# Optimization experiments

Measured on AMD Instinct MI355X. Metric: run time of the kernel, lower is better.

Reference implementation:

```python
import jax, jax.numpy as jnp
import numpy as np

D_HEAD = 64
IGNORE = -100000.0


def setup_inputs() -> dict:
    key = jax.random.key(0)
    ks = jax.random.split(key, 5)
    B, S, D, H, M = 2, 2048, 768, 12, D_HEAD
    scale = 0.05  # 'random_normal' keras init stddev
    return {
        "x": jax.random.normal(ks[0], (B, S, D), jnp.float32),
        "W_Q": jax.random.normal(ks[1], (H, D, M), jnp.float32) * scale,
        "b_Q": jnp.zeros((H, M), jnp.float32),
        "W_K": jax.random.normal(ks[2], (H, D, M), jnp.float32) * scale,
        "b_K": jnp.zeros((H, M), jnp.float32),
        "W_V": jax.random.normal(ks[3], (H, D, M), jnp.float32) * scale,
        "b_V": jnp.zeros((H, M), jnp.float32),
        "W_O": jax.random.normal(ks[4], (H, M, D), jnp.float32) * scale,
        "b_O": jnp.zeros((D,), jnp.float32),
    }


def reference(x, W_Q, b_Q, W_K, b_K, W_V, b_V, W_O, b_O):
    # q,k,v: [b, s, h, m]
    q = jnp.einsum("bqd,hdm->bqhm", x, W_Q) + b_Q
    k = jnp.einsum("bkd,hdm->bkhm", x, W_K) + b_K
    v = jnp.einsum("bkd,hdm->bkhm", x, W_V) + b_V
    # scores: [b, h, q, k], scaled by 1/sqrt(d_head)
    scores = jnp.einsum("bqhm,bkhm->bhqk", q, k) / jnp.sqrt(
        jnp.asarray(D_HEAD, q.dtype)
    )
    S = x.shape[1]
    # causal mask: strictly-upper-triangular positions set to IGNORE (-1e5),
    # matching tf.where(mask == 1, IGNORE, scores)
    causal = jnp.arange(S)[:, None] >= jnp.arange(S)[None, :]  # [q, k]
    scores = jnp.where(causal[None, None, :, :], scores, jnp.asarray(IGNORE, scores.dtype))
    pattern = jax.nn.softmax(scores, axis=-1)
    z = jnp.einsum("bhqk,bkhm->bqhm", pattern, v)
    attn_out = jnp.einsum("bqhm,hmd->bqd", z, W_O) + b_O
    return attn_out
```

## Files before the change

### kernel.cpp

```cpp
#include <hip/hip_runtime.h>
#include <hip/hip_bf16.h>
#include <cstdint>
#include <cstddef>

#define B_ 2
#define S_ 2048
#define D_ 768
#define H_ 12
#define M_ 64
#define BS_ (B_ * S_)
#define NQKV_ 2304
#define NCHUNK_ 80
#define TOTCHUNK_ (24 * NCHUNK_)
#define QSCALE 0.18033688011f

typedef __attribute__((ext_vector_type(8))) short bf16x8;
typedef __attribute__((ext_vector_type(4))) short bf16x4;
typedef __attribute__((ext_vector_type(4))) float f32x4;

__device__ __forceinline__ unsigned short f2bu(float f) {
    __hip_bfloat16 h = __float2bfloat16(f);
    unsigned short u;
    __builtin_memcpy(&u, &h, 2);
    return u;
}
__device__ __forceinline__ unsigned pack2(float a, float b) {
    return (unsigned)f2bu(a) | ((unsigned)f2bu(b) << 16);
}

__device__ __forceinline__ bf16x8 ld16(const unsigned short* p) {
    p = (const unsigned short*)__builtin_assume_aligned(p, 16);
    bf16x8 v; __builtin_memcpy(&v, p, 16); return v;
}
__device__ __forceinline__ bf16x4 ld8(const unsigned short* p) {
    p = (const unsigned short*)__builtin_assume_aligned(p, 8);
    bf16x4 v; __builtin_memcpy(&v, p, 8); return v;
}
__device__ __forceinline__ uint4 ld16u(const unsigned short* p) {
    p = (const unsigned short*)__builtin_assume_aligned(p, 16);
    uint4 v; __builtin_memcpy(&v, p, 16); return v;
}
__device__ __forceinline__ void st16(unsigned short* p, uint4 v) {
    p = (unsigned short*)__builtin_assume_aligned(p, 16);
    __builtin_memcpy(p, &v, 16);
}
__device__ __forceinline__ void st8(unsigned short* p, uint2 v) {
    p = (unsigned short*)__builtin_assume_aligned(p, 8);
    __builtin_memcpy(p, &v, 8);
}
__device__ __forceinline__ float4 ldf4(const float* p) {
    p = (const float*)__builtin_assume_aligned(p, 16);
    float4 v; __builtin_memcpy(&v, p, 16); return v;
}
__device__ __forceinline__ void async16(const unsigned short* g, unsigned short* l) {
    __builtin_amdgcn_global_load_lds(
        (const __attribute__((address_space(1))) void*)g,
        (__attribute__((address_space(3))) void*)l, 16, 0, 0);
}
__device__ __forceinline__ void b82f(uint4 u, float* o) {
    o[0] = __uint_as_float(u.x << 16); o[1] = __uint_as_float(u.x & 0xffff0000u);
    o[2] = __uint_as_float(u.y << 16); o[3] = __uint_as_float(u.y & 0xffff0000u);
    o[4] = __uint_as_float(u.z << 16); o[5] = __uint_as_float(u.z & 0xffff0000u);
    o[6] = __uint_as_float(u.w << 16); o[7] = __uint_as_float(u.w & 0xffff0000u);
}

#define NEG_BIG (-3.0e38f)

__global__ void prep(const float* __restrict__ WQ, const float* __restrict__ WK,
                     const float* __restrict__ WV, const float* __restrict__ WO,
                     const float* __restrict__ x,
                     unsigned short* __restrict__ WT,
                     unsigned short* __restrict__ WOT,
                     unsigned short* __restrict__ xb)
{
    const int bx = blockIdx.x;
    if (bx < 216) {
        const int xx = bx % 9, yy = bx / 9;
        const int c  = xx * 256 + threadIdx.x;
        const int k0 = yy * 32;
        const int which = c / D_;
        const int r = c - which * D_;
        const int h = r >> 6, m = r & 63;
        const float* Wsel = (which == 0) ? WQ : (which == 1) ? WK : WV;
        const float* src = Wsel + (size_t)h * D_ * M_ + m;
        unsigned short* dst = WT + (size_t)c * D_ + k0;
        for (int i = 0; i < 32; i += 8) {
            float wv[8];
#pragma unroll
            for (int j = 0; j < 8; j++) wv[j] = src[(size_t)(k0 + i + j) * M_];
            uint4 pu;
            pu.x = pack2(wv[0], wv[1]); pu.y = pack2(wv[2], wv[3]);
            pu.z = pack2(wv[4], wv[5]); pu.w = pack2(wv[6], wv[7]);
            st16(dst + i, pu);
        }
    } else if (bx < 288) {
        const int b2 = bx - 216;
        const int xx = b2 % 3, yy = b2 / 3;
        const int c  = xx * 256 + threadIdx.x;
        const int k0 = yy * 32;
        unsigned short* dst = WOT + (size_t)c * D_ + k0;
        for (int i = 0; i < 32; i += 8) {
            float wv[8];
#pragma unroll
            for (int j = 0; j < 8; j++) wv[j] = WO[(size_t)(k0 + i + j) * D_ + c];
            uint4 pu;
            pu.x = pack2(wv[0], wv[1]); pu.y = pack2(wv[2], wv[3]);
            pu.z = pack2(wv[4], wv[5]); pu.w = pack2(wv[6], wv[7]);
            st16(dst + i, pu);
        }
    } else {
        const size_t i = ((size_t)(bx - 288) * 256 + threadIdx.x) * 16;
#pragma unroll
        for (int p = 0; p < 2; p++) {
            float4 a0 = ldf4(x + i + p * 8), a1 = ldf4(x + i + p * 8 + 4);
            uint4 u;
            u.x = pack2(a0.x, a0.y); u.y = pack2(a0.z, a0.w);
            u.z = pack2(a1.x, a1.y); u.w = pack2(a1.z, a1.w);
            st16(xb + i + p * 8, u);
        }
    }
}

__global__ __launch_bounds__(256, 2) void qkv_gemm(
    const unsigned short* __restrict__ xb,
    const unsigned short* __restrict__ WT,
    const float* __restrict__ bQ, const float* __restrict__ bK,
    const float* __restrict__ bV,
    unsigned short* __restrict__ qo, unsigned short* __restrict__ ko,
    unsigned short* __restrict__ vt)
{
    const int row0 = blockIdx.x * 128;
    const int col0 = blockIdx.y * 128;
    const int t = threadIdx.x;
    const int w = t >> 6, lane = t & 63, quad = lane >> 4, l16 = lane & 15;
    const int wrow0 = (w & 1) * 64, wcol0 = (w >> 1) * 64;

    __shared__ unsigned short Alds[128 * 64];
    __shared__ unsigned short Blds[128 * 64];

    f32x4 acc[4][4] = {};

    const unsigned short* asrc[4];
    const unsigned short* bsrc[4];
    int ldsoff[4];
#pragma unroll
    for (int q = 0; q < 4; q++) {
        const int cq = w * 256 + q * 64 + lane;
        const int row = cq >> 3, c = cq & 7;
        const int cs = c ^ (row & 7);
        asrc[q] = xb + (size_t)(row0 + row) * D_ + cs * 8;
        bsrc[q] = WT + (size_t)(col0 + row) * D_ + cs * 8;
        ldsoff[q] = (w * 256 + q * 64) * 8;
    }
    const int swz = (l16 & 7);

    for (int k0 = 0; k0 < D_; k0 += 64) {
#pragma unroll
        for (int q = 0; q < 4; q++) async16(asrc[q] + k0, Alds + ldsoff[q]);
#pragma unroll
        for (int q = 0; q < 4; q++) async16(bsrc[q] + k0, Blds + ldsoff[q]);
        __syncthreads();

        bf16x8 af[4][2], bfm[4][2];
#pragma unroll
        for (int rt = 0; rt < 4; rt++) {
            const int row = wrow0 + rt * 16 + l16;
#pragma unroll
            for (int hh = 0; hh < 2; hh++)
                af[rt][hh] = ld16(&Alds[row * 64 + ((hh * 4 + quad) ^ swz) * 8]);
        }
#pragma unroll
        for (int st = 0; st < 4; st++) {
            const int row = wcol0 + st * 16 + l16;
#pragma unroll
            for (int hh = 0; hh < 2; hh++)
                bfm[st][hh] = ld16(&Blds[row * 64 + ((hh * 4 + quad) ^ swz) * 8]);
        }
#pragma unroll
        for (int rt = 0; rt < 4; rt++)
#pragma unroll
            for (int st = 0; st < 4; st++) {
                acc[rt][st] = __builtin_amdgcn_mfma_f32_16x16x32_bf16(
                    af[rt][0], bfm[st][0], acc[rt][st], 0, 0, 0);
                acc[rt][st] = __builtin_amdgcn_mfma_f32_16x16x32_bf16(
                    af[rt][1], bfm[st][1], acc[rt][st], 0, 0, 0);
            }
        __syncthreads();
    }

    const int which = col0 / D_;
    const int colin = col0 - which * D_;

    if (which == 0) {
#pragma unroll
        for (int st = 0; st < 4; st++) {
            const int cl = colin + wcol0 + st * 16 + l16;
            const int h = cl >> 6, m = cl & 63;
            const float bval = bQ[cl];
#pragma unroll
            for (int rt = 0; rt < 4; rt++)
#pragma unroll
                for (int rr = 0; rr < 4; rr++) {
                    const int R = row0 + wrow0 + rt * 16 + quad * 4 + rr;
                    const int bb = R >> 11, s = R & (S_ - 1);
                    qo[(((size_t)bb * H_ + h) * S_ + s) * M_ + m] =
                        f2bu((acc[rt][st][rr] + bval) * QSCALE);
                }
        }
    } else if (which == 1) {
#pragma unroll
        for (int st = 0; st < 4; st++) {
            const int cl = colin + wcol0 + st * 16 + l16;
            const int h = cl >> 6, m = cl & 63;
            const int blk = m >> 3, inn = m & 7;
            const float bval = bK[cl];
#pragma unroll
            for (int rt = 0; rt < 4; rt++)
#pragma unroll
                for (int rr = 0; rr < 4; rr++) {
                    const int R = row0 + wrow0 + rt * 16 + quad * 4 + rr;
                    const int bb = R >> 11, s = R & (S_ - 1);
                    ko[(((size_t)bb * H_ + h) * S_ + s) * M_ +
                       ((blk ^ (s & 7)) << 3) + inn] =
                        f2bu(acc[rt][st][rr] + bval);
                }
        }
    } else {
#pragma unroll
        for (int st = 0; st < 4; st++) {
            const int cl = colin + wcol0 + st * 16 + l16;
            const int h = cl >> 6, m = cl & 63;
            const float bval = bV[cl];
#pragma unroll
            for (int rt = 0; rt < 4; rt++) {
                const int R0 = row0 + wrow0 + rt * 16 + quad * 4;
                const int bb = R0 >> 11, s0 = R0 & (S_ - 1);
                const int tile = s0 >> 7;
                const int gl = (s0 & 127) >> 2;
                const int pl = gl >> 1, hi = gl & 1;
                const int pp = pl ^ ((m >> 1) & 7);
                const int half = hi ^ (m & 1);
                uint2 v;
                v.x = pack2(acc[rt][st][0] + bval, acc[rt][st][1] + bval);
                v.y = pack2(acc[rt][st][2] + bval, acc[rt][st][3] + bval);
                st8(&vt[(((size_t)bb * H_ + h) * 16 + tile) * (M_ * 128)
                        + m * 128 + (pp * 2 + half) * 4], v);
            }
        }
    }
}

__global__ __launch_bounds__(256, 2) void attn_split(
    const unsigned short* __restrict__ Q,
    const unsigned short* __restrict__ Kin,
    const unsigned short* __restrict__ Vt,
    unsigned short* __restrict__ Opart,
    float* __restrict__ ml)
{
    const int flat = blockIdx.y * NCHUNK_ + blockIdx.x;
    const int bh = flat % 24;
    const int xx = (NCHUNK_ - 1) - flat / 24;

    int qt, c, nc;
    if (xx < 8)       { qt = xx; c = 0; nc = 1; }
    else if (xx < 24) { int u = xx - 8;  qt = 8  + (u >> 1); c = u & 1;  nc = 2; }
    else if (xx < 48) { int u = xx - 24; qt = 16 + u / 3;    c = u % 3;  nc = 3; }
    else              { int u = xx - 48; qt = 24 + (u >> 2); c = u & 3;  nc = 4; }

    const int ci     = bh * NCHUNK_ + xx;
    const int kbeg   = c * 512;
    const int keyend = min((qt + 1) * 64, kbeg + 512);
    const int iters  = (keyend - kbeg + 127) >> 7;
    const bool lastchunk = (c == nc - 1);

    const int t = threadIdx.x;
    const int wave = t >> 6, lane = t & 63, quad = lane >> 4, l16 = lane & 15;

    const unsigned short* Qb  = Q   + ((size_t)bh * S_ + qt * 64) * M_;
    const unsigned short* Kb  = Kin + (size_t)bh * S_ * M_;
    const unsigned short* Vb  = Vt  + (size_t)bh * M_ * S_;

    __shared__ unsigned short Klds[128 * 64];
    __shared__ unsigned short Vlds[64 * 128];

    bf16x8 qf[2];
    {
        const unsigned short* qrow = Qb + (size_t)(wave * 16 + l16) * M_;
        qf[0] = ld16(qrow + quad * 8);
        qf[1] = ld16(qrow + 32 + quad * 8);
    }

    const int ksw = l16 & 7;
    const int ko0 = (quad ^ ksw) * 8;
    const int ko1 = ((quad + 4) ^ ksw) * 8;
    int voff[8];
#pragma unroll
    for (int st = 0; st < 8; st++)
        voff[st] = l16 * 128 + (quad ^ (l16 & 3)) * 4
                 + ((st ^ ((l16 >> 2) & 3)) << 4);

    const int wdst = wave * 64 * 8;

    f32x4 o_acc[4] = {};
    float lrow = 0.f;

    for (int it = 0; it < iters; it++) {
        __syncthreads();
        const int key0 = kbeg + it * 128;
        const unsigned short* kt = Kb + (size_t)key0 * M_;
        const unsigned short* vtile = Vb + (size_t)(key0 >> 7) * (M_ * 128);
#pragma unroll
        for (int q = 0; q < 4; q++)
            async16(kt + (size_t)(q * 256 + t) * 8, Klds + q * 2048 + wdst);
#pragma unroll
        for (int q = 0; q < 4; q++)
            async16(vtile + (size_t)(q * 256 + t) * 8, Vlds + q * 2048 + wdst);
        __syncthreads();

        f32x4 s_acc[8];
#pragma unroll
        for (int st = 0; st < 8; st++) {
            f32x4 z4 = {0.f, 0.f, 0.f, 0.f};
            const unsigned short* krow = &Klds[(st * 16 + l16) * 64];
            bf16x8 k0 = ld16(krow + ko0);
            bf16x8 k1 = ld16(krow + ko1);
            z4 = __builtin_amdgcn_mfma_f32_16x16x32_bf16(k0, qf[0], z4, 0, 0, 0);
            z4 = __builtin_amdgcn_mfma_f32_16x16x32_bf16(k1, qf[1], z4, 0, 0, 0);
            s_acc[st] = z4;
        }

        if (lastchunk && it == iters - 1) {
            const int keyq = kbeg + it * 128 + quad * 4;
            const int qg = qt * 64 + wave * 16 + l16;
#pragma unroll
            for (int st = 0; st < 8; st++)
#pragma unroll
                for (int r = 0; r < 4; r++)
                    if (keyq + st * 16 + r > qg)
                        s_acc[st][r] = -1e30f;
        }

        bf16x4 pkv[8];
#pragma unroll
        for (int st = 0; st < 8; st++) {
            float p0 = exp2f(s_acc[st][0]);
            float p1 = exp2f(s_acc[st][1]);
            float p2 = exp2f(s_acc[st][2]);
            float p3 = exp2f(s_acc[st][3]);
            lrow += (p0 + p1) + (p2 + p3);
            uint2 u;
            u.x = pack2(p0, p1);
            u.y = pack2(p2, p3);
            __builtin_memcpy(&pkv[st], &u, 8);
        }

#pragma unroll
        for (int stf = 0; stf < 4; stf++) {
#pragma unroll
            for (int st = 0; st < 8; st++) {
                bf16x4 va = ld8(&Vlds[stf * 2048 + voff[st]]);
                o_acc[stf] = __builtin_amdgcn_mfma_f32_16x16x16bf16_1k(
                    va, pkv[st], o_acc[stf], 0, 0, 0);
            }
        }
    }

    lrow += __shfl_xor(lrow, 16, 64);
    lrow += __shfl_xor(lrow, 32, 64);

    unsigned short* Op = Opart + (size_t)ci * 4096;
    const int q = wave * 16 + l16;
#pragma unroll
    for (int stf = 0; stf < 4; stf++) {
        uint2 u;
        u.x = pack2(o_acc[stf][0], o_acc[stf][1]);
        u.y = pack2(o_acc[stf][2], o_acc[stf][3]);
        st8(&Op[q * 64 + stf * 16 + quad * 4], u);
    }
    if (quad == 0)
        ml[(size_t)ci * 128 + 64 + q] = lrow;
}

__global__ void combine(const unsigned short* __restrict__ Opart,
                        const float* __restrict__ ml,
                        unsigned short* __restrict__ Z)
{
    const int qt = blockIdx.x, bh = blockIdx.y;
    const int b = bh / H_, h = bh - b * H_;
    const int g = qt >> 3, r7 = qt & 7;
    const int nc = g + 1;
    const int base = bh * NCHUNK_ + qt + 4 * g * (g - 1) + r7 * g;

    const int t = threadIdx.x;
    const int q = t >> 2, fs = (t & 3) * 16;

    float L = 0.f;
    for (int c = 0; c < nc; c++)
        L += ml[(size_t)(base + c) * 128 + 64 + q];
    const float invL = 1.0f / L;

    float o[16] = {};
    for (int c = 0; c < nc; c++) {
        const unsigned short* op =
            Opart + (size_t)(base + c) * 4096 + q * 64 + fs;
        float f[8];
        b82f(ld16u(op), f);
#pragma unroll
        for (int j = 0; j < 8; j++) o[j] += f[j];
        b82f(ld16u(op + 8), f);
#pragma unroll
        for (int j = 0; j < 8; j++) o[8 + j] += f[j];
    }

    unsigned short* zp =
        Z + ((size_t)b * S_ + qt * 64 + q) * (H_ * M_) + h * M_ + fs;
    uint4 u0, u1;
    u0.x = pack2(o[0]*invL,  o[1]*invL);  u0.y = pack2(o[2]*invL,  o[3]*invL);
    u0.z = pack2(o[4]*invL,  o[5]*invL);  u0.w = pack2(o[6]*invL,  o[7]*invL);
    u1.x = pack2(o[8]*invL,  o[9]*invL);  u1.y = pack2(o[10]*invL, o[11]*invL);
    u1.z = pack2(o[12]*invL, o[13]*invL); u1.w = pack2(o[14]*invL, o[15]*invL);
    st16(zp, u0);
    st16(zp + 8, u1);
}

__global__ __launch_bounds__(256, 2) void oproj_gemm(
    const unsigned short* __restrict__ Zin,
    const unsigned short* __restrict__ WOT,
    const float* __restrict__ bO,
    float* __restrict__ out)
{
    const int row0 = blockIdx.x * 128;
    const int col0 = blockIdx.y * 128;
    const int t = threadIdx.x;
    const int w = t >> 6, lane = t & 63, quad = lane >> 4, l16 = lane & 15;
    const int wrow0 = (w & 1) * 64, wcol0 = (w >> 1) * 64;

    __shared__ unsigned short Alds[128 * 64];
    __shared__ unsigned short Blds[128 * 64];

    f32x4 acc[4][4] = {};

    const unsigned short* asrc[4];
    const unsigned short* bsrc[4];
    int ldsoff[4];
#pragma unroll
    for (int q = 0; q < 4; q++) {
        const int cq = w * 256 + q * 64 + lane;
        const int row = cq >> 3, c = cq & 7;
        const int cs = c ^ (row & 7);
        asrc[q] = Zin + (size_t)(row0 + row) * D_ + cs * 8;
        bsrc[q] = WOT + (size_t)(col0 + row) * D_ + cs * 8;
        ldsoff[q] = (w * 256 + q * 64) * 8;
    }
    const int swz = (l16 & 7);

    for (int k0 = 0; k0 < D_; k0 += 64) {
#pragma unroll
        for (int q = 0; q < 4; q++) async16(asrc[q] + k0, Alds + ldsoff[q]);
#pragma unroll
        for (int q = 0; q < 4; q++) async16(bsrc[q] + k0, Blds + ldsoff[q]);
        __syncthreads();

        bf16x8 af[4][2], bfm[4][2];
#pragma unroll
        for (int rt = 0; rt < 4; rt++) {
            const int row = wrow0 + rt * 16 + l16;
#pragma unroll
            for (int hh = 0; hh < 2; hh++)
                af[rt][hh] = ld16(&Alds[row * 64 + ((hh * 4 + quad) ^ swz) * 8]);
        }
#pragma unroll
        for (int st = 0; st < 4; st++) {
            const int row = wcol0 + st * 16 + l16;
#pragma unroll
            for (int hh = 0; hh < 2; hh++)
                bfm[st][hh] = ld16(&Blds[row * 64 + ((hh * 4 + quad) ^ swz) * 8]);
        }
#pragma unroll
        for (int rt = 0; rt < 4; rt++)
#pragma unroll
            for (int st = 0; st < 4; st++) {
                acc[rt][st] = __builtin_amdgcn_mfma_f32_16x16x32_bf16(
                    af[rt][0], bfm[st][0], acc[rt][st], 0, 0, 0);
                acc[rt][st] = __builtin_amdgcn_mfma_f32_16x16x32_bf16(
                    af[rt][1], bfm[st][1], acc[rt][st], 0, 0, 0);
            }
        __syncthreads();
    }

#pragma unroll
    for (int st = 0; st < 4; st++) {
        const int c = col0 + wcol0 + st * 16 + l16;
        const float bval = bO[c];
#pragma unroll
        for (int rt = 0; rt < 4; rt++)
#pragma unroll
            for (int rr = 0; rr < 4; rr++) {
                const int R = row0 + wrow0 + rt * 16 + quad * 4 + rr;
                out[(size_t)R * D_ + c] = acc[rt][st][rr] + bval;
            }
    }
}

extern "C" void kernel_launch(void* const* d_in, const int* in_sizes, int n_in,
                              void* d_out, int out_size, void* d_ws, size_t ws_size,
                              hipStream_t stream)
{
    const float* x  = (const float*)d_in[0];
    const float* WQ = (const float*)d_in[1];
    const float* bQ = (const float*)d_in[2];
    const float* WK = (const float*)d_in[3];
    const float* bK = (const float*)d_in[4];
    const float* WV = (const float*)d_in[5];
    const float* bV = (const float*)d_in[6];
    const float* WO = (const float*)d_in[7];
    const float* bO = (const float*)d_in[8];
    float* out = (float*)d_out;

    const size_t n = (size_t)B_ * H_ * S_ * M_;
    unsigned short* q_ws  = (unsigned short*)d_ws;
    unsigned short* k_ws  = q_ws + n;
    unsigned short* vt_ws = k_ws + n;
    unsigned short* z_ws  = vt_ws + n;
    unsigned short* WT    = z_ws + n;
    unsigned short* WOT   = WT + (size_t)NQKV_ * D_;
    unsigned short* xb    = WOT + (size_t)D_ * D_;
    unsigned short* Opart = xb + (size_t)BS_ * D_;
    float* mlbuf = (float*)(Opart + (size_t)TOTCHUNK_ * 4096);

    prep<<<dim3(1056), 256, 0, stream>>>(WQ, WK, WV, WO, x, WT, WOT, xb);
    qkv_gemm<<<dim3(BS_ / 128, NQKV_ / 128), 256, 0, stream>>>(
        xb, WT, bQ, bK, bV, q_ws, k_ws, vt_ws);
    attn_split<<<dim3(NCHUNK_, B_ * H_), 256, 0, stream>>>(
        q_ws, k_ws, vt_ws, Opart, mlbuf);
    combine<<<dim3(S_ / 64, B_ * H_), 256, 0, stream>>>(Opart, mlbuf, z_ws);
    oproj_gemm<<<dim3(BS_ / 128, D_ / 128), 256, 0, stream>>>(
        z_ws, WOT, bO, out);
}
```

Measured before the change: 158.3 us.

## Double-buffer LDS tiles in QKV and output-projection GEMMs to overlap loads

Both projection GEMMs now use two LDS buffers per operand. The next K-tile's async global-to-LDS copy is issued right after the barrier, while the current tile is being computed, and the trailing __syncthreads is removed. The goal is to hide global load latency behind the MFMA work. LDS use doubles to 64KB per block, which could limit the two-blocks-per-CU occupancy on some configurations, and the single barrier per iteration must be enough to prevent write-after-read races on the buffer being refilled.

Measured after the change: 171.3 us. 8.2% more time.

```diff
diff --git a/kernel.cpp b/kernel.cpp
--- a/kernel.cpp
+++ b/kernel.cpp
@@ -135,8 +135,8 @@
     const int w = t >> 6, lane = t & 63, quad = lane >> 4, l16 = lane & 15;
     const int wrow0 = (w & 1) * 64, wcol0 = (w >> 1) * 64;
 
-    __shared__ unsigned short Alds[128 * 64];
-    __shared__ unsigned short Blds[128 * 64];
+    __shared__ unsigned short Alds[2][128 * 64];
+    __shared__ unsigned short Blds[2][128 * 64];
 
     f32x4 acc[4][4] = {};
 
@@ -154,12 +154,27 @@
     }
     const int swz = (l16 & 7);
 
-    for (int k0 = 0; k0 < D_; k0 += 64) {
-#pragma unroll
-        for (int q = 0; q < 4; q++) async16(asrc[q] + k0, Alds + ldsoff[q]);
-#pragma unroll
-        for (int q = 0; q < 4; q++) async16(bsrc[q] + k0, Blds + ldsoff[q]);
-        __syncthreads();
+    auto stageg = [&](int it) {
+        const int k0 = it * 64;
+        unsigned short* ad = Alds[it & 1];
+        unsigned short* bd = Blds[it & 1];
+#pragma unroll
+        for (int q = 0; q < 4; q++) async16(asrc[q] + k0, ad + ldsoff[q]);
+#pragma unroll
+        for (int q = 0; q < 4; q++) async16(bsrc[q] + k0, bd + ldsoff[q]);
+    };
+
+    stageg(0);
+
+    for (int it = 0; it < D_ / 64; it++) {
+        asm volatile("s_waitcnt vmcnt(0)" ::: "memory");
+        __builtin_amdgcn_s_barrier();
+        __builtin_amdgcn_sched_barrier(0);
+
+        if (it + 1 < D_ / 64) stageg(it + 1);
+
+        const unsigned short* Al = Alds[it & 1];
+        const unsigned short* Bl = Blds[it & 1];
 
         bf16x8 af[4][2], bfm[4][2];
 #pragma unroll
@@ -167,14 +182,14 @@
             const int row = wrow0 + rt * 16 + l16;
 #pragma unroll
             for (int hh = 0; hh < 2; hh++)
-                af[rt][hh] = ld16(&Alds[row * 64 + ((hh * 4 + quad) ^ swz) * 8]);
+                af[rt][hh] = ld16(&Al[row * 64 + ((hh * 4 + quad) ^ swz) * 8]);
         }
 #pragma unroll
         for (int st = 0; st < 4; st++) {
             const int row = wcol0 + st * 16 + l16;
 #pragma unroll
             for (int hh = 0; hh < 2; hh++)
-                bfm[st][hh] = ld16(&Blds[row * 64 + ((hh * 4 + quad) ^ swz) * 8]);
+                bfm[st][hh] = ld16(&Bl[row * 64 + ((hh * 4 + quad) ^ swz) * 8]);
         }
 #pragma unroll
         for (int rt = 0; rt < 4; rt++)
@@ -185,7 +200,6 @@
                 acc[rt][st] = __builtin_amdgcn_mfma_f32_16x16x32_bf16(
                     af[rt][1], bfm[st][1], acc[rt][st], 0, 0, 0);
             }
-        __syncthreads();
     }
 
     const int which = col0 / D_;
@@ -435,8 +449,8 @@
     const int w = t >> 6, lane = t & 63, quad = lane >> 4, l16 = lane & 15;
     const int wrow0 = (w & 1) * 64, wcol0 = (w >> 1) * 64;
 
-    __shared__ unsigned short Alds[128 * 64];
-    __shared__ unsigned short Blds[128 * 64];
+    __shared__ unsigned short Alds[2][128 * 64];
+    __shared__ unsigned short Blds[2][128 * 64];
 
     f32x4 acc[4][4] = {};
 
@@ -454,12 +468,27 @@
     }
     const int swz = (l16 & 7);
 
-    for (int k0 = 0; k0 < D_; k0 += 64) {
-#pragma unroll
-        for (int q = 0; q < 4; q++) async16(asrc[q] + k0, Alds + ldsoff[q]);
-#pragma unroll
-        for (int q = 0; q < 4; q++) async16(bsrc[q] + k0, Blds + ldsoff[q]);
-        __syncthreads();
+    auto stageg = [&](int it) {
+        const int k0 = it * 64;
+        unsigned short* ad = Alds[it & 1];
+        unsigned short* bd = Blds[it & 1];
+#pragma unroll
+        for (int q = 0; q < 4; q++) async16(asrc[q] + k0, ad + ldsoff[q]);
+#pragma unroll
+        for (int q = 0; q < 4; q++) async16(bsrc[q] + k0, bd + ldsoff[q]);
+    };
+
+    stageg(0);
+
+    for (int it = 0; it < D_ / 64; it++) {
+        asm volatile("s_waitcnt vmcnt(0)" ::: "memory");
+        __builtin_amdgcn_s_barrier();
+        __builtin_amdgcn_sched_barrier(0);
+
+        if (it + 1 < D_ / 64) stageg(it + 1);
+
+        const unsigned short* Al = Alds[it & 1];
+        const unsigned short* Bl = Blds[it & 1];
 
         bf16x8 af[4][2], bfm[4][2];
 #pragma unroll
@@ -467,14 +496,14 @@
             const int row = wrow0 + rt * 16 + l16;
 #pragma unroll
             for (int hh = 0; hh < 2; hh++)
-                af[rt][hh] = ld16(&Alds[row * 64 + ((hh * 4 + quad) ^ swz) * 8]);
+                af[rt][hh] = ld16(&Al[row * 64 + ((hh * 4 + quad) ^ swz) * 8]);
         }
 #pragma unroll
         for (int st = 0; st < 4; st++) {
             const int row = wcol0 + st * 16 + l16;
 #pragma unroll
             for (int hh = 0; hh < 2; hh++)
-                bfm[st][hh] = ld16(&Blds[row * 64 + ((hh * 4 + quad) ^ swz) * 8]);
+                bfm[st][hh] = ld16(&Bl[row * 64 + ((hh * 4 + quad) ^ swz) * 8]);
         }
 #pragma unroll
         for (int rt = 0; rt < 4; rt++)
@@ -485,7 +514,6 @@
                 acc[rt][st] = __builtin_amdgcn_mfma_f32_16x16x32_bf16(
                     af[rt][1], bfm[st][1], acc[rt][st], 0, 0, 0);
             }
-        __syncthreads();
     }
 
 #pragma unroll
```
